# Optimization experiments

Measured on AMD Instinct MI355X. Metric: run time of the kernel, lower is better.

Reference implementation:

```python
import jax, jax.numpy as jnp
import numpy as np
from jax import lax

# Dims
HID = 2048          # hidden_size
DI = 4096           # d_inner = expand * hidden
NH = 64             # mamba heads
P = 64              # head dim
N = 128             # d_state
G = 1               # n_groups
K = 4               # conv kernel
IM = 8192           # MLP intermediate
BB, L = 2, 2048
EPS = 1e-5
CONV_DIM = DI + 2 * G * N            # 4352
D_IN_PROJ = 2 * DI + 2 * G * N + NH  # 8512


def rmsnorm(x, w, eps=EPS):
    v = jnp.mean(jnp.square(x), axis=-1, keepdims=True)
    return x * jax.lax.rsqrt(v + eps) * w


def setup_inputs() -> dict:
    key = jax.random.key(0)
    ks = jax.random.split(key, 16)
    s = 0.02
    return {
        "positions": jnp.broadcast_to(jnp.arange(L, dtype=jnp.int32), (BB, L)),
        "hidden_states": jax.random.normal(ks[0], (BB, L, HID), jnp.float32),
        "residual": jax.random.normal(ks[1], (BB, L, HID), jnp.float32),
        "in_proj_w": jax.random.normal(ks[2], (D_IN_PROJ, HID), jnp.float32) * s,
        "conv_w": jax.random.normal(ks[3], (CONV_DIM, K), jnp.float32) * 0.2,
        "conv_b": jax.random.normal(ks[4], (CONV_DIM,), jnp.float32) * 0.02,
        "A_log": jnp.log(jnp.arange(1, NH + 1, dtype=jnp.float32)),
        "D": jnp.ones((NH,), jnp.float32),
        "dt_bias": jax.random.uniform(ks[5], (NH,), jnp.float32, -4.0, -2.0),
        "mixer_norm_w": jnp.ones((DI,), jnp.float32),
        "out_proj_w": jax.random.normal(ks[6], (HID, DI), jnp.float32) * s,
        "input_ln_w": jnp.ones((HID,), jnp.float32),
        "pre_ff_ln_w": jnp.ones((HID,), jnp.float32),
        "gate_up_w": jax.random.normal(ks[7], (2 * IM, HID), jnp.float32) * s,
        "down_w": jax.random.normal(ks[8], (HID, IM), jnp.float32) * s,
    }


def reference(positions, hidden_states, residual, in_proj_w, conv_w, conv_b,
              A_log, D, dt_bias, mixer_norm_w, out_proj_w, input_ln_w,
              pre_ff_ln_w, gate_up_w, down_w):
    del positions  # not used by the mamba mixer math
    B_, Lq, _ = hidden_states.shape

    # --- input RMSNorm with fused residual add ---
    residual = hidden_states + residual
    hs = rmsnorm(residual, input_ln_w)

    # --- Mamba2 mixer ---
    proj = jnp.einsum('bld,ed->ble', hs, in_proj_w)   # [B,L,D_IN_PROJ]
    z = proj[..., :DI]
    xBC = proj[..., DI:DI + CONV_DIM]
    dt = proj[..., DI + CONV_DIM:]                    # [B,L,NH]

    # causal depthwise conv (kernel K) + SiLU
    xp = jnp.pad(xBC, ((0, 0), (K - 1, 0), (0, 0)))
    conv = conv_b
    for k in range(K):
        conv = conv + xp[:, k:k + Lq, :] * conv_w[:, k]
    xBC = jax.nn.silu(conv)

    x = xBC[..., :DI].reshape(B_, Lq, NH, P)
    Bm = xBC[..., DI:DI + G * N].reshape(B_, Lq, G, N)
    Cm = xBC[..., DI + G * N:].reshape(B_, Lq, G, N)
    rep = NH // G
    Bm = jnp.repeat(Bm, rep, axis=2)                  # [B,L,NH,N]
    Cm = jnp.repeat(Cm, rep, axis=2)

    dt = jax.nn.softplus(dt + dt_bias)                # [B,L,NH]
    A = -jnp.exp(A_log)                               # [NH]
    dA = jnp.exp(dt * A)                              # [B,L,NH]

    def step(h, inp):
        x_t, B_t, C_t, dA_t, dt_t = inp               # [B,NH,P],[B,NH,N],[B,NH,N],[B,NH],[B,NH]
        h = dA_t[..., None, None] * h + \
            (dt_t[..., None, None] * x_t[..., None]) * B_t[:, :, None, :]
        y = jnp.einsum('bhpn,bhn->bhp', h, C_t)
        return h, y

    xs = (x.transpose(1, 0, 2, 3), Bm.transpose(1, 0, 2, 3),
          Cm.transpose(1, 0, 2, 3), dA.transpose(1, 0, 2), dt.transpose(1, 0, 2))
    h0 = jnp.zeros((B_, NH, P, N), hidden_states.dtype)
    _, ys = lax.scan(step, h0, xs)                    # [L,B,NH,P]
    y = ys.transpose(1, 0, 2, 3) + D[None, None, :, None] * x
    y = y.reshape(B_, Lq, DI)

    # gated RMSNorm (Mixer2RMSNormGated, n_groups=1)
    y = y * jax.nn.silu(z)
    y = rmsnorm(y, mixer_norm_w)
    mamba_out = jnp.einsum('bld,hd->blh', y, out_proj_w)

    # --- pre-FF RMSNorm with fused residual add ---
    residual2 = mamba_out + residual
    hs2 = rmsnorm(residual2, pre_ff_ln_w)

    # --- gated MLP (SiluAndMul) ---
    gu = jnp.einsum('bld,ed->ble', hs2, gate_up_w)    # [B,L,2*IM]
    act = jax.nn.silu(gu[..., :IM]) * gu[..., IM:]
    out = jnp.einsum('bli,hi->blh', act, down_w)
    return out, residual2
```

## Files before the change

kernel.cpp:

```cpp
#include <hip/hip_runtime.h>

#define T_TOK 4096
#define HID   2048
#define DI    4096
#define NH    64
#define PDIM  64
#define NSTATE 128
#define IM    8192
#define LSEQ  2048
#define CONVD 4352
#define DPROJ 8512
#define DPADR 8704
#define QC    64
#define NCH   32

typedef __bf16 bf16x8 __attribute__((ext_vector_type(8)));
typedef float  f32x4  __attribute__((ext_vector_type(4)));

__device__ __forceinline__ unsigned short f2bf(float f) {
  unsigned u = __float_as_uint(f);
  u = (u + 0x7fffu + ((u >> 16) & 1u)) >> 16;
  return (unsigned short)u;
}
__device__ __forceinline__ float bf2f(unsigned short h) {
  return __uint_as_float(((unsigned)h) << 16);
}
__device__ __forceinline__ float siluf(float x) {
  return x / (1.f + __expf(-x));
}

#define GLL(gaddr, laddr) __builtin_amdgcn_global_load_lds( \
    (const __attribute__((address_space(1))) void*)(gaddr), \
    (__attribute__((address_space(3))) void*)(laddr), 16, 0, 0)

__global__ __launch_bounds__(256) void k_cvt(const float* __restrict__ src,
                                             unsigned short* __restrict__ dst, int n4) {
  int gid = blockIdx.x * 256 + threadIdx.x;
  if (gid >= n4) return;
  float4 v = *(const float4*)&src[(size_t)gid * 4];
  unsigned short* o = dst + (size_t)gid * 4;
  o[0] = f2bf(v.x); o[1] = f2bf(v.y); o[2] = f2bf(v.z); o[3] = f2bf(v.w);
}

__global__ __launch_bounds__(256) void k_cvt_inproj(const float* __restrict__ src,
                                                    unsigned short* __restrict__ dst) {
  int gid = blockIdx.x * 256 + threadIdx.x;
  size_t idx4 = (size_t)gid * 4;
  int r = (int)(idx4 >> 11);
  unsigned short* o = dst + idx4;
  if (r < DPROJ) {
    float4 v = *(const float4*)&src[(size_t)r * HID + (idx4 & 2047)];
    o[0] = f2bf(v.x); o[1] = f2bf(v.y); o[2] = f2bf(v.z); o[3] = f2bf(v.w);
  } else {
    o[0] = 0; o[1] = 0; o[2] = 0; o[3] = 0;
  }
}

__global__ __launch_bounds__(256) void k_cvt_gu(const float* __restrict__ src,
                                                unsigned short* __restrict__ dst) {
  int gid = blockIdx.x * 256 + threadIdx.x;
  size_t idx4 = (size_t)gid * 4;
  int r = (int)(idx4 >> 11), k = (int)(idx4 & 2047);
  int g = r >> 6, j = r & 63;
  int srcr = (j < 32) ? (g * 32 + j) : (IM + g * 32 + (j - 32));
  float4 v = *(const float4*)&src[(size_t)srcr * HID + k];
  unsigned short* o = dst + idx4;
  o[0] = f2bf(v.x); o[1] = f2bf(v.y); o[2] = f2bf(v.z); o[3] = f2bf(v.w);
}

template <int EPI, int BM>
__global__ __launch_bounds__(512, 2)
void gemm8(const unsigned short* __restrict__ A, const unsigned short* __restrict__ W,
           int K, int ntn, int ldo, void* __restrict__ outp,
           const float* __restrict__ resid) {
  (void)ntn;
  constexpr int MREP  = BM / 32;
  constexpr int ABYT  = BM * 128;
  constexpr int BUFB  = ABYT + 32768;
  constexpr int NTM   = 4096 / BM;
  __shared__ __align__(16) char smem[2 * BUFB];
  const int t = threadIdx.x;
  const int w = t >> 6, l = t & 63;
  const int lr = l & 15, hi = l >> 4;
  const int wr = w >> 2, wc = w & 3;

  const int q = (int)gridDim.x >> 3;
  const int bid = blockIdx.x;
  const int id2 = (bid & 7) * q + (bid >> 3);
  const int tn = id2 / NTM, tm = id2 % NTM;
  const int m0b = tm * BM, n0b = tn << 8;

  const int srow = t >> 3;
  const int scole = ((t & 7) << 3) ^ ((t & 32) ? 16 : 0) ^ ((t & 64) ? 32 : 0);
  const unsigned short* Ag = A + (size_t)(m0b + srow) * K + scole;
  const unsigned short* Wg = W + (size_t)(n0b + srow) * K + scole;
  const int ldsw = w * 1024;

  const int fa = ((lr & 4) ? 32 : 0) | ((lr & 8) ? 64 : 0);
  const int arow = (wr * (BM / 2) + lr) * 128 + hi * 16;
  const int brow = (wc * 64 + lr) * 128 + hi * 16;
  const int aoff0 = arow ^ fa, aoff1 = (arow + 64) ^ fa;
  const int boff0 = brow ^ fa, boff1 = (brow + 64) ^ fa;

#define ISSUE_A(jt, bb) do {                                                    \
    _Pragma("unroll")                                                           \
    for (int p_ = 0; p_ < BM / 64; ++p_)                                        \
      GLL(Ag + (size_t)(p_ * 64) * K + (size_t)(jt) * 64,                       \
          smem + (bb) * BUFB + p_ * 8192 + ldsw); } while (0)
#define ISSUE_B(jt, bb) do {                                                    \
    _Pragma("unroll")                                                           \
    for (int p_ = 0; p_ < 4; ++p_)                                              \
      GLL(Wg + (size_t)(p_ * 64) * K + (size_t)(jt) * 64,                       \
          smem + (bb) * BUFB + ABYT + p_ * 8192 + ldsw); } while (0)

#define RDF(off, base) (*(const bf16x8*)((base) + (off)))
#define MF(P, x, y, c0, c1, c2, c3) do {                                                     \
    __builtin_amdgcn_s_setprio(1);                                                           \
    acc[2*(P)  ][0] = __builtin_amdgcn_mfma_f32_16x16x32_bf16((x),(c0),acc[2*(P)  ][0],0,0,0);\
    acc[2*(P)+1][0] = __builtin_amdgcn_mfma_f32_16x16x32_bf16((y),(c0),acc[2*(P)+1][0],0,0,0);\
    acc[2*(P)  ][1] = __builtin_amdgcn_mfma_f32_16x16x32_bf16((x),(c1),acc[2*(P)  ][1],0,0,0);\
    acc[2*(P)+1][1] = __builtin_amdgcn_mfma_f32_16x16x32_bf16((y),(c1),acc[2*(P)+1][1],0,0,0);\
    acc[2*(P)  ][2] = __builtin_amdgcn_mfma_f32_16x16x32_bf16((x),(c2),acc[2*(P)  ][2],0,0,0);\
    acc[2*(P)+1][2] = __builtin_amdgcn_mfma_f32_16x16x32_bf16((y),(c2),acc[2*(P)+1][2],0,0,0);\
    acc[2*(P)  ][3] = __builtin_amdgcn_mfma_f32_16x16x32_bf16((x),(c3),acc[2*(P)  ][3],0,0,0);\
    acc[2*(P)+1][3] = __builtin_amdgcn_mfma_f32_16x16x32_bf16((y),(c3),acc[2*(P)+1][3],0,0,0);\
    __builtin_amdgcn_s_setprio(0); } while (0)

  f32x4 acc[MREP][4];
#pragma unroll
  for (int m = 0; m < MREP; m++)
#pragma unroll
    for (int n = 0; n < 4; n++) acc[m][n] = (f32x4){0.f, 0.f, 0.f, 0.f};

  const int nkt = K >> 6;
  ISSUE_A(0, 0); ISSUE_B(0, 0);

  for (int j = 0; j < nkt; ++j) {
    const int cur = j & 1;
    const char* Ab = smem + cur * BUFB;
    const char* Bb = Ab + ABYT;
    asm volatile("s_waitcnt vmcnt(0)" ::: "memory");
    __builtin_amdgcn_s_barrier();
    __builtin_amdgcn_sched_barrier(0);
    if (j + 1 < nkt) { ISSUE_A(j + 1, cur ^ 1); ISSUE_B(j + 1, cur ^ 1); }
    bf16x8 b0 = RDF(boff0, Bb), b1 = RDF(boff0 + 2048, Bb),
           b2 = RDF(boff0 + 4096, Bb), b3 = RDF(boff0 + 6144, Bb);
    bf16x8 af0 = RDF(aoff0, Ab), af1 = RDF(aoff0 + 2048, Ab);
    bf16x8 af2, af3, b4, b5, b6, b7;
    if constexpr (MREP == 8) {
      af2 = RDF(aoff0 + 4096, Ab); af3 = RDF(aoff0 + 6144, Ab);
      MF(0, af0, af1, b0, b1, b2, b3);
      af0 = RDF(aoff0 + 8192, Ab); af1 = RDF(aoff0 + 10240, Ab);
      MF(1, af2, af3, b0, b1, b2, b3);
      af2 = RDF(aoff0 + 12288, Ab); af3 = RDF(aoff0 + 14336, Ab);
      MF(2, af0, af1, b0, b1, b2, b3);
      b4 = RDF(boff1, Bb); b5 = RDF(boff1 + 2048, Bb);
      b6 = RDF(boff1 + 4096, Bb); b7 = RDF(boff1 + 6144, Bb);
      af0 = RDF(aoff1, Ab); af1 = RDF(aoff1 + 2048, Ab);
      MF(3, af2, af3, b0, b1, b2, b3);
      af2 = RDF(aoff1 + 4096, Ab); af3 = RDF(aoff1 + 6144, Ab);
      MF(0, af0, af1, b4, b5, b6, b7);
      af0 = RDF(aoff1 + 8192, Ab); af1 = RDF(aoff1 + 10240, Ab);
      MF(1, af2, af3, b4, b5, b6, b7);
      af2 = RDF(aoff1 + 12288, Ab); af3 = RDF(aoff1 + 14336, Ab);
      MF(2, af0, af1, b4, b5, b6, b7);
      MF(3, af2, af3, b4, b5, b6, b7);
    } else {
      af2 = RDF(aoff0 + 4096, Ab); af3 = RDF(aoff0 + 6144, Ab);
      MF(0, af0, af1, b0, b1, b2, b3);
      b4 = RDF(boff1, Bb); b5 = RDF(boff1 + 2048, Bb);
      b6 = RDF(boff1 + 4096, Bb); b7 = RDF(boff1 + 6144, Bb);
      af0 = RDF(aoff1, Ab); af1 = RDF(aoff1 + 2048, Ab);
      MF(1, af2, af3, b0, b1, b2, b3);
      af2 = RDF(aoff1 + 4096, Ab); af3 = RDF(aoff1 + 6144, Ab);
      MF(0, af0, af1, b4, b5, b6, b7);
      MF(1, af2, af3, b4, b5, b6, b7);
    }
  }

  if constexpr (EPI == 0) {
    unsigned short* op = (unsigned short*)outp;
#pragma unroll
    for (int m = 0; m < MREP; m++)
#pragma unroll
      for (int n = 0; n < 4; n++)
#pragma unroll
        for (int r = 0; r < 4; r++) {
          int row = m0b + wr * (BM / 2) + m * 16 + hi * 4 + r;
          int col = n0b + wc * 64 + n * 16 + lr;
          op[(size_t)row * ldo + col] = f2bf(acc[m][n][r]);
        }
  } else if constexpr (EPI == 2) {
    unsigned short* op = (unsigned short*)outp;
    const int gbase = (n0b + wc * 64) >> 1;
#pragma unroll
    for (int m = 0; m < MREP; m++)
#pragma unroll
      for (int n = 0; n < 2; n++)
#pragma unroll
        for (int r = 0; r < 4; r++) {
          int row = m0b + wr * (BM / 2) + m * 16 + hi * 4 + r;
          int col = gbase + n * 16 + lr;
          float g = acc[m][n][r], u = acc[m][n + 2][r];
          op[(size_t)row * ldo + col] = f2bf(siluf(g) * u);
        }
  } else {
    float* op = (float*)outp;
#pragma unroll
    for (int m = 0; m < MREP; m++)
#pragma unroll
      for (int n = 0; n < 4; n++)
#pragma unroll
        for (int r = 0; r < 4; r++) {
          int row = m0b + wr * (BM / 2) + m * 16 + hi * 4 + r;
          int col = n0b + wc * 64 + n * 16 + lr;
          float v = acc[m][n][r];
          if constexpr (EPI == 1) v += resid[(size_t)row * ldo + col];
          op[(size_t)row * ldo + col] = v;
        }
  }
#undef ISSUE_A
#undef ISSUE_B
#undef RDF
#undef MF
}

__device__ __forceinline__ float block_reduce_sum256(float v, float* sred) {
#pragma unroll
  for (int m = 32; m; m >>= 1) v += __shfl_xor(v, m);
  int t = threadIdx.x;
  if ((t & 63) == 0) sred[t >> 6] = v;
  __syncthreads();
  return sred[0] + sred[1] + sred[2] + sred[3];
}

__global__ __launch_bounds__(256)
void k_addnorm(const float* __restrict__ hin, const float* __restrict__ rin,
               const float* __restrict__ wln, float* __restrict__ rout,
               unsigned short* __restrict__ hbf) {
  __shared__ float sred[4];
  const int tok = blockIdx.x, t = threadIdx.x;
  const size_t base = (size_t)tok * HID + t * 8;
  float4 a0 = *(const float4*)&hin[base];
  float4 a1 = *(const float4*)&hin[base + 4];
  float4 b0 = *(const float4*)&rin[base];
  float4 b1 = *(const float4*)&rin[base + 4];
  float v[8] = {a0.x + b0.x, a0.y + b0.y, a0.z + b0.z, a0.w + b0.w,
                a1.x + b1.x, a1.y + b1.y, a1.z + b1.z, a1.w + b1.w};
  float ss = 0.f;
#pragma unroll
  for (int j = 0; j < 8; j++) ss += v[j] * v[j];
  float tot = block_reduce_sum256(ss, sred);
  float rms = rsqrtf(tot * (1.f / HID) + 1e-5f);
  *(float4*)&rout[base] = (float4){v[0], v[1], v[2], v[3]};
  *(float4*)&rout[base + 4] = (float4){v[4], v[5], v[6], v[7]};
  float4 w0 = *(const float4*)&wln[t * 8];
  float4 w1 = *(const float4*)&wln[t * 8 + 4];
  float wa[8] = {w0.x, w0.y, w0.z, w0.w, w1.x, w1.y, w1.z, w1.w};
  unsigned short o[8];
#pragma unroll
  for (int j = 0; j < 8; j++) o[j] = f2bf(v[j] * rms * wa[j]);
  *(ushort4*)&hbf[base] = *(ushort4*)&o[0];
  *(ushort4*)&hbf[base + 4] = *(ushort4*)&o[4];
}

__global__ __launch_bounds__(256)
void k_rmsnorm_bf(const float* __restrict__ src, const float* __restrict__ wln,
                  unsigned short* __restrict__ dst) {
  __shared__ float sred[4];
  const int tok = blockIdx.x, t = threadIdx.x;
  const size_t base = (size_t)tok * HID + t * 8;
  float4 a0 = *(const float4*)&src[base];
  float4 a1 = *(const float4*)&src[base + 4];
  float v[8] = {a0.x, a0.y, a0.z, a0.w, a1.x, a1.y, a1.z, a1.w};
  float ss = 0.f;
#pragma unroll
  for (int j = 0; j < 8; j++) ss += v[j] * v[j];
  float tot = block_reduce_sum256(ss, sred);
  float rms = rsqrtf(tot * (1.f / HID) + 1e-5f);
  float4 w0 = *(const float4*)&wln[t * 8];
  float4 w1 = *(const float4*)&wln[t * 8 + 4];
  float wa[8] = {w0.x, w0.y, w0.z, w0.w, w1.x, w1.y, w1.z, w1.w};
  unsigned short o[8];
#pragma unroll
  for (int j = 0; j < 8; j++) o[j] = f2bf(v[j] * rms * wa[j]);
  *(ushort4*)&dst[base] = *(ushort4*)&o[0];
  *(ushort4*)&dst[base + 4] = *(ushort4*)&o[4];
}

__global__ __launch_bounds__(256)
void k_gatenorm(const unsigned short* __restrict__ ybuf, const unsigned short* __restrict__ projbf,
                const float* __restrict__ wmix, unsigned short* __restrict__ ynorm) {
  __shared__ float sred[4];
  const int tok = blockIdx.x, t = threadIdx.x;
  const size_t yb = (size_t)tok * DI;
  const size_t pb = (size_t)tok * DPADR;
  float g[16];
  float ss = 0.f;
#pragma unroll
  for (int j = 0; j < 16; j++) {
    int idx = j * 256 + t;
    float yv = bf2f(ybuf[yb + idx]);
    float z = bf2f(projbf[pb + idx]);
    float gg = yv * siluf(z);
    g[j] = gg;
    ss += gg * gg;
  }
  float tot = block_reduce_sum256(ss, sred);
  float rms = rsqrtf(tot * (1.f / DI) + 1e-5f);
#pragma unroll
  for (int j = 0; j < 16; j++) {
    int idx = j * 256 + t;
    ynorm[yb + idx] = f2bf(g[j] * rms * wmix[idx]);
  }
}

__global__ __launch_bounds__(256)
void k_conv(const unsigned short* __restrict__ projbf, const float* __restrict__ cw,
            const float* __restrict__ cb, unsigned short* __restrict__ xbf,
            unsigned short* __restrict__ bcbf) {
  const int c = blockIdx.x * 256 + threadIdx.x;
  const int tk = blockIdx.y;
  const int lpos = tk & (LSEQ - 1);
  float4 wv = *(const float4*)&cw[c * 4];
  float wk[4] = {wv.x, wv.y, wv.z, wv.w};
  float acc = cb[c];
#pragma unroll
  for (int k = 0; k < 4; k++) {
    int lp = lpos - 3 + k;
    if (lp >= 0) acc += bf2f(projbf[(size_t)(tk - 3 + k) * DPADR + DI + c]) * wk[k];
  }
  unsigned short r = f2bf(siluf(acc));
  if (c < DI) xbf[(size_t)tk * DI + c] = r;
  else        bcbf[(size_t)tk * 256 + (c - DI)] = r;
}

__global__ __launch_bounds__(256)
void k_dt(const unsigned short* __restrict__ projbf, const float* __restrict__ dt_bias,
          float* __restrict__ dtg) {
  int gid = blockIdx.x * 256 + threadIdx.x;
  int tk = gid >> 6, hh = gid & 63;
  float x = bf2f(projbf[(size_t)tk * DPADR + (DI + CONVD) + hh]) + dt_bias[hh];
  float dt = (x > 20.f) ? x : log1pf(__expf(x));
  dtg[gid] = dt;
}

__global__ __launch_bounds__(256)
void k_ssd1(const unsigned short* __restrict__ xbf, const unsigned short* __restrict__ bcbf,
            const float* __restrict__ dtg, const float* __restrict__ A_log,
            const float* __restrict__ Dv, unsigned short* __restrict__ ybuf,
            unsigned short* __restrict__ Sc, float* __restrict__ dtsum) {
  __shared__ __align__(16) char smem[60928];
  unsigned short* sBs  = (unsigned short*)(smem);
  unsigned short* sCs  = (unsigned short*)(smem + 16384);
  unsigned short* sMs  = (unsigned short*)(smem + 16384);
  unsigned short* sBsT = (unsigned short*)(smem + 32768);
  unsigned short* sXsT = (unsigned short*)(smem + 51200);
  float* sdt = (float*)(smem + 60416);
  float* sdl = (float*)(smem + 60672);

  const int bi = blockIdx.x;
  const int ch = bi & 31, h = (bi >> 5) & 63, b = bi >> 11;
  const int bh = b * NH + h;
  const int tok0 = b * LSEQ + ch * QC;
  const int t = threadIdx.x;
  const int w = t >> 6, l = t & 63, lr = l & 15, hi = l >> 4;
  const float Ah = -__expf(A_log[h]);
  const float Dh = Dv[h];

  {
    const int srow = t >> 4, scol = (t & 15) * 8;
#pragma unroll
    for (int i = 0; i < 4; i++) {
      const unsigned short* gb = bcbf + (size_t)(tok0 + srow + 16 * i) * 256 + scol;
      GLL(gb, (char*)sBs + i * 4096 + w * 1024);
      GLL(gb + 128, (char*)sCs + i * 4096 + w * 1024);
    }
  }
  if (t < QC) sdt[t] = dtg[(size_t)(tok0 + t) * NH + h];
  __syncthreads();
  if (t < QC) sdl[t] = sdt[t];
  __syncthreads();
  for (int off = 1; off < QC; off <<= 1) {
    float v = 0.f;
    if (t < QC && t >= off) v = sdl[t - off];
    __syncthreads();
    if (t < QC) sdl[t] += v;
    __syncthreads();
  }

  {
    const int s = t >> 2;
    const float DlQ = sdl[QC - 1];
    const float csc = __expf(Ah * (DlQ - sdl[s])) * sdt[s];
    const int n0 = (t & 3) * 32;
#pragma unroll
    for (int j = 0; j < 32; j++) {
      float bv = bf2f(sBs[s * 128 + n0 + j]);
      sBsT[(n0 + j) * 72 + s] = f2bf(csc * bv);
    }
    const int p0 = (t & 3) * 16;
    const unsigned short* gx = xbf + (size_t)(tok0 + s) * DI + h * 64 + p0;
    union { uint4 v; unsigned short u[8]; } x0, x1;
    x0.v = *(const uint4*)gx;
    x1.v = *(const uint4*)(gx + 8);
#pragma unroll
    for (int j = 0; j < 8; j++) {
      sXsT[(p0 + j) * 72 + s] = x0.u[j];
      sXsT[(p0 + 8 + j) * 72 + s] = x1.u[j];
    }
  }
  __syncthreads();

  f32x4 accS[4];
#pragma unroll
  for (int jf = 0; jf < 4; jf++) accS[jf] = (f32x4){0.f, 0.f, 0.f, 0.f};
#pragma unroll
  for (int ks = 0; ks < 4; ks++) {
    bf16x8 a = *(const bf16x8*)&sBs[(w * 16 + lr) * 128 + ks * 32 + hi * 8];
#pragma unroll
    for (int jf = 0; jf < 4; jf++) {
      bf16x8 bb = *(const bf16x8*)&sCs[(jf * 16 + lr) * 128 + ks * 32 + hi * 8];
      accS[jf] = __builtin_amdgcn_mfma_f32_16x16x32_bf16(a, bb, accS[jf], 0, 0, 0);
    }
  }
  __syncthreads();

  {
    const int s0 = w * 16 + hi * 4;
#pragma unroll
    for (int jf = 0; jf < 4; jf++) {
      const int tt = jf * 16 + lr;
      const float dlt = sdl[tt];
      unsigned short mv[4];
#pragma unroll
      for (int r = 0; r < 4; r++) {
        const int ss = s0 + r;
        float val = 0.f;
        if (ss <= tt) val = accS[jf][r] * __expf(Ah * (dlt - sdl[ss])) * sdt[ss];
        mv[r] = f2bf(val);
      }
      *(ushort4*)&sMs[tt * 72 + s0] = *(ushort4*)mv;
    }
  }
  __syncthreads();

  {
    f32x4 accY[4];
#pragma unroll
    for (int jf = 0; jf < 4; jf++) accY[jf] = (f32x4){0.f, 0.f, 0.f, 0.f};
#pragma unroll
    for (int ks = 0; ks < 2; ks++) {
      bf16x8 a = *(const bf16x8*)&sMs[(w * 16 + lr) * 72 + ks * 32 + hi * 8];
#pragma unroll
      for (int jf = 0; jf < 4; jf++) {
        bf16x8 bb = *(const bf16x8*)&sXsT[(jf * 16 + lr) * 72 + ks * 32 + hi * 8];
        accY[jf] = __builtin_amdgcn_mfma_f32_16x16x32_bf16(a, bb, accY[jf], 0, 0, 0);
      }
    }
#pragma unroll
    for (int jf = 0; jf < 4; jf++)
#pragma unroll
      for (int r = 0; r < 4; r++) {
        const int tt = w * 16 + hi * 4 + r;
        const int pp = jf * 16 + lr;
        float xv = bf2f(sXsT[pp * 72 + tt]);
        ybuf[(size_t)(tok0 + tt) * DI + h * 64 + pp] = f2bf(accY[jf][r] + Dh * xv);
      }
  }

  {
    f32x4 accT[8];
#pragma unroll
    for (int jf = 0; jf < 8; jf++) accT[jf] = (f32x4){0.f, 0.f, 0.f, 0.f};
#pragma unroll
    for (int ks = 0; ks < 2; ks++) {
      bf16x8 a = *(const bf16x8*)&sXsT[(w * 16 + lr) * 72 + ks * 32 + hi * 8];
#pragma unroll
      for (int jf = 0; jf < 8; jf++) {
        bf16x8 bb = *(const bf16x8*)&sBsT[(jf * 16 + lr) * 72 + ks * 32 + hi * 8];
        accT[jf] = __builtin_amdgcn_mfma_f32_16x16x32_bf16(a, bb, accT[jf], 0, 0, 0);
      }
    }
    unsigned short* sc = Sc + ((size_t)bh * NCH + ch) * (PDIM * NSTATE);
#pragma unroll
    for (int jf = 0; jf < 8; jf++)
#pragma unroll
      for (int r = 0; r < 4; r++) {
        const int pp = w * 16 + hi * 4 + r;
        const int nn = jf * 16 + lr;
        sc[pp * NSTATE + nn] = f2bf(accT[jf][r]);
      }
  }
  if (t == 0) dtsum[bh * NCH + ch] = sdl[QC - 1];
}

__global__ __launch_bounds__(256)
void k_ssd2(const float* __restrict__ A_log, const float* __restrict__ dtsum,
            unsigned short* __restrict__ ScHt) {
  const int blk = blockIdx.x;
  const int bh = blk >> 3, pg = blk & 7;
  const int t = threadIdx.x;
  const int p = pg * 8 + (t >> 5), n0 = (t & 31) * 4;
  const int h = bh & 63;
  const float Ah = -__expf(A_log[h]);
  float H[4] = {0.f, 0.f, 0.f, 0.f};
  for (int c = 0; c < NCH; c++) {
    size_t base = (((size_t)bh * NCH + c) * PDIM + p) * NSTATE + n0;
    ushort4 sv = *(const ushort4*)&ScHt[base];
    float dec = __expf(Ah * dtsum[bh * NCH + c]);
    ushort4 hv;
    hv.x = f2bf(H[0]); hv.y = f2bf(H[1]); hv.z = f2bf(H[2]); hv.w = f2bf(H[3]);
    *(ushort4*)&ScHt[base] = hv;
    H[0] = dec * H[0] + bf2f(sv.x);
    H[1] = dec * H[1] + bf2f(sv.y);
    H[2] = dec * H[2] + bf2f(sv.z);
    H[3] = dec * H[3] + bf2f(sv.w);
  }
}

__global__ __launch_bounds__(256)
void k_ssd3(const unsigned short* __restrict__ bcbf, const unsigned short* __restrict__ Ht,
            const float* __restrict__ dtg, const float* __restrict__ A_log,
            unsigned short* __restrict__ ybuf) {
  __shared__ __align__(16) char smem[33280];
  unsigned short* sCs = (unsigned short*)(smem);
  unsigned short* sHt = (unsigned short*)(smem + 16384);
  float* sdt = (float*)(smem + 32768);
  float* sdl = (float*)(smem + 33024);

  const int bi = blockIdx.x;
  const int ch = bi & 31, h = (bi >> 5) & 63, b = bi >> 11;
  const int bh = b * NH + h;
  const int tok0 = b * LSEQ + ch * QC;
  const int t = threadIdx.x;
  const int w = t >> 6, l = t & 63, lr = l & 15, hi = l >> 4;
  const float Ah = -__expf(A_log[h]);

  {
    const int srow = t >> 4, scol = (t & 15) * 8;
    const unsigned short* gh = Ht + ((size_t)bh * NCH + ch) * (PDIM * NSTATE);
#pragma unroll
    for (int i = 0; i < 4; i++) {
      const unsigned short* gc = bcbf + (size_t)(tok0 + srow + 16 * i) * 256 + 128 + scol;
      GLL(gc, (char*)sCs + i * 4096 + w * 1024);
      GLL(gh + i * 2048 + t * 8, (char*)sHt + i * 4096 + w * 1024);
    }
  }
  if (t < QC) sdt[t] = dtg[(size_t)(tok0 + t) * NH + h];
  __syncthreads();
  if (t < QC) sdl[t] = sdt[t];
  __syncthreads();
  for (int off = 1; off < QC; off <<= 1) {
    float v = 0.f;
    if (t < QC && t >= off) v = sdl[t - off];
    __syncthreads();
    if (t < QC) sdl[t] += v;
    __syncthreads();
  }

  f32x4 acc[4];
#pragma unroll
  for (int jf = 0; jf < 4; jf++) acc[jf] = (f32x4){0.f, 0.f, 0.f, 0.f};
#pragma unroll
  for (int ks = 0; ks < 4; ks++) {
    bf16x8 a = *(const bf16x8*)&sCs[(w * 16 + lr) * 128 + ks * 32 + hi * 8];
#pragma unroll
    for (int jf = 0; jf < 4; jf++) {
      bf16x8 bb = *(const bf16x8*)&sHt[(jf * 16 + lr) * 128 + ks * 32 + hi * 8];
      acc[jf] = __builtin_amdgcn_mfma_f32_16x16x32_bf16(a, bb, acc[jf], 0, 0, 0);
    }
  }
#pragma unroll
  for (int jf = 0; jf < 4; jf++)
#pragma unroll
    for (int r = 0; r < 4; r++) {
      const int tt = w * 16 + hi * 4 + r;
      const int pp = jf * 16 + lr;
      const float dec = __expf(Ah * sdl[tt]);
      const size_t o = (size_t)(tok0 + tt) * DI + h * 64 + pp;
      ybuf[o] = f2bf(bf2f(ybuf[o]) + dec * acc[jf][r]);
    }
}

static const size_t OFF_WBF_IN  = 0;
static const size_t OFF_WBF_OUT = 35651584;
static const size_t OFF_WBF_GU  = 52428800;
static const size_t OFF_WBF_DN  = 119537664;
static const size_t OFF_RESID   = 153092096;
static const size_t OFF_HSBF    = 186646528;
static const size_t OFF_PROJ    = 203423744;
static const size_t OFF_XBF     = 274726912;
static const size_t OFF_BCBF    = 308281344;
static const size_t OFF_DTG     = 310378496;
static const size_t OFF_YBUF    = 311427072;
static const size_t OFF_SC      = 344981504;
static const size_t OFF_DTSUM   = 412090368;

extern "C" void kernel_launch(void* const* d_in, const int* in_sizes, int n_in,
                              void* d_out, int out_size, void* d_ws, size_t ws_size,
                              hipStream_t stream) {
  (void)in_sizes; (void)n_in; (void)out_size; (void)ws_size;
  const float* hidden   = (const float*)d_in[1];
  const float* resin    = (const float*)d_in[2];
  const float* w_inproj = (const float*)d_in[3];
  const float* conv_w   = (const float*)d_in[4];
  const float* conv_b   = (const float*)d_in[5];
  const float* A_log    = (const float*)d_in[6];
  const float* Dvec     = (const float*)d_in[7];
  const float* dt_bias  = (const float*)d_in[8];
  const float* w_mix    = (const float*)d_in[9];
  const float* w_outp   = (const float*)d_in[10];
  const float* w_ln1    = (const float*)d_in[11];
  const float* w_ln2    = (const float*)d_in[12];
  const float* w_gu     = (const float*)d_in[13];
  const float* w_dn     = (const float*)d_in[14];

  char* ws = (char*)d_ws;
  unsigned short* wbf_in  = (unsigned short*)(ws + OFF_WBF_IN);
  unsigned short* wbf_out = (unsigned short*)(ws + OFF_WBF_OUT);
  unsigned short* wbf_gu  = (unsigned short*)(ws + OFF_WBF_GU);
  unsigned short* wbf_dn  = (unsigned short*)(ws + OFF_WBF_DN);
  float*          residb  = (float*)(ws + OFF_RESID);
  unsigned short* hsbf    = (unsigned short*)(ws + OFF_HSBF);
  unsigned short* projbf  = (unsigned short*)(ws + OFF_PROJ);
  unsigned short* actbf   = (unsigned short*)(ws + OFF_PROJ);
  unsigned short* xbf     = (unsigned short*)(ws + OFF_XBF);
  unsigned short* ynormbf = (unsigned short*)(ws + OFF_XBF);
  unsigned short* bcbf    = (unsigned short*)(ws + OFF_BCBF);
  float*          dtgb    = (float*)(ws + OFF_DTG);
  unsigned short* ybuf    = (unsigned short*)(ws + OFF_YBUF);
  unsigned short* scht    = (unsigned short*)(ws + OFF_SC);
  float*          dtsumb  = (float*)(ws + OFF_DTSUM);

  float* out0 = (float*)d_out;
  float* res2 = out0 + (size_t)T_TOK * HID;

  k_cvt_inproj<<<17408, 256, 0, stream>>>(w_inproj, wbf_in);
  k_cvt<<<8192, 256, 0, stream>>>(w_outp, wbf_out, 2097152);
  k_cvt_gu<<<32768, 256, 0, stream>>>(w_gu, wbf_gu);
  k_cvt<<<16384, 256, 0, stream>>>(w_dn, wbf_dn, 4194304);

  k_addnorm<<<T_TOK, 256, 0, stream>>>(hidden, resin, w_ln1, residb, hsbf);
  gemm8<0, 256><<<34 * 16, 512, 0, stream>>>(hsbf, wbf_in, HID, 34, DPADR, projbf, nullptr);
  k_conv<<<dim3(17, T_TOK), 256, 0, stream>>>(projbf, conv_w, conv_b, xbf, bcbf);
  k_dt<<<T_TOK * NH / 256, 256, 0, stream>>>(projbf, dt_bias, dtgb);
  k_ssd1<<<4096, 256, 0, stream>>>(xbf, bcbf, dtgb, A_log, Dvec, ybuf, scht, dtsumb);
  k_ssd2<<<1024, 256, 0, stream>>>(A_log, dtsumb, scht);
  k_ssd3<<<4096, 256, 0, stream>>>(bcbf, scht, dtgb, A_log, ybuf);
  k_gatenorm<<<T_TOK, 256, 0, stream>>>(ybuf, projbf, w_mix, ynormbf);
  gemm8<1, 128><<<8 * 32, 512, 0, stream>>>(ynormbf, wbf_out, DI, 8, HID, res2, residb);
  k_rmsnorm_bf<<<T_TOK, 256, 0, stream>>>(res2, w_ln2, hsbf);
  gemm8<2, 256><<<64 * 16, 512, 0, stream>>>(hsbf, wbf_gu, HID, 64, IM, actbf, nullptr);
  gemm8<3, 128><<<8 * 32, 512, 0, stream>>>(actbf, wbf_dn, IM, 8, HID, out0, nullptr);
}
```

Before: 1.007 ms.

## Restructure GEMM main loop into barrier-separated phases with split global prefetch

The GEMM inner loop is rewritten into NQ phases per k-tile. In each phase the LDS fragment reads are issued first, then the next tile's global-to-LDS loads (A in the first phase, B in the second for the large tile), then a barrier and a block of MFMAs at raised priority, with the vmcnt wait deferred to the last phase. The aim is to keep waves in lockstep and spread memory issue across the compute so loads overlap with MFMA work better. In exchange it adds more barriers per k-tile and changes register pressure, since all eight B fragments are loaded up front.

Result: slower. 1.064 ms (+5.7%).

```diff
diff --git a/kernel.cpp b/kernel.cpp
--- a/kernel.cpp
+++ b/kernel.cpp
@@ -71,10 +71,10 @@
 template <int EPI, int BM>
 __global__ __launch_bounds__(512, 2)
 void gemm8(const unsigned short* __restrict__ A, const unsigned short* __restrict__ W,
-           int K, int ntn, int ldo, void* __restrict__ outp,
+           int K, int ldo, void* __restrict__ outp,
            const float* __restrict__ resid) {
-  (void)ntn;
   constexpr int MREP  = BM / 32;
+  constexpr int NQ    = MREP / 2;
   constexpr int ABYT  = BM * 128;
   constexpr int BUFB  = ABYT + 32768;
   constexpr int NTM   = 4096 / BM;
@@ -84,9 +84,9 @@
   const int lr = l & 15, hi = l >> 4;
   const int wr = w >> 2, wc = w & 3;
 
-  const int q = (int)gridDim.x >> 3;
+  const int q8 = (int)gridDim.x >> 3;
   const int bid = blockIdx.x;
-  const int id2 = (bid & 7) * q + (bid >> 3);
+  const int id2 = (bid & 7) * q8 + (bid >> 3);
   const int tn = id2 / NTM, tm = id2 % NTM;
   const int m0b = tm * BM, n0b = tn << 8;
 
@@ -114,17 +114,6 @@
           smem + (bb) * BUFB + ABYT + p_ * 8192 + ldsw); } while (0)
 
 #define RDF(off, base) (*(const bf16x8*)((base) + (off)))
-#define MF(P, x, y, c0, c1, c2, c3) do {                                                     \
-    __builtin_amdgcn_s_setprio(1);                                                           \
-    acc[2*(P)  ][0] = __builtin_amdgcn_mfma_f32_16x16x32_bf16((x),(c0),acc[2*(P)  ][0],0,0,0);\
-    acc[2*(P)+1][0] = __builtin_amdgcn_mfma_f32_16x16x32_bf16((y),(c0),acc[2*(P)+1][0],0,0,0);\
-    acc[2*(P)  ][1] = __builtin_amdgcn_mfma_f32_16x16x32_bf16((x),(c1),acc[2*(P)  ][1],0,0,0);\
-    acc[2*(P)+1][1] = __builtin_amdgcn_mfma_f32_16x16x32_bf16((y),(c1),acc[2*(P)+1][1],0,0,0);\
-    acc[2*(P)  ][2] = __builtin_amdgcn_mfma_f32_16x16x32_bf16((x),(c2),acc[2*(P)  ][2],0,0,0);\
-    acc[2*(P)+1][2] = __builtin_amdgcn_mfma_f32_16x16x32_bf16((y),(c2),acc[2*(P)+1][2],0,0,0);\
-    acc[2*(P)  ][3] = __builtin_amdgcn_mfma_f32_16x16x32_bf16((x),(c3),acc[2*(P)  ][3],0,0,0);\
-    acc[2*(P)+1][3] = __builtin_amdgcn_mfma_f32_16x16x32_bf16((y),(c3),acc[2*(P)+1][3],0,0,0);\
-    __builtin_amdgcn_s_setprio(0); } while (0)
 
   f32x4 acc[MREP][4];
 #pragma unroll
@@ -134,47 +123,51 @@
 
   const int nkt = K >> 6;
   ISSUE_A(0, 0); ISSUE_B(0, 0);
+  asm volatile("s_waitcnt vmcnt(0)" ::: "memory");
+  __builtin_amdgcn_s_barrier();
+  __builtin_amdgcn_sched_barrier(0);
 
   for (int j = 0; j < nkt; ++j) {
     const int cur = j & 1;
     const char* Ab = smem + cur * BUFB;
     const char* Bb = Ab + ABYT;
-    asm volatile("s_waitcnt vmcnt(0)" ::: "memory");
-    __builtin_amdgcn_s_barrier();
-    __builtin_amdgcn_sched_barrier(0);
-    if (j + 1 < nkt) { ISSUE_A(j + 1, cur ^ 1); ISSUE_B(j + 1, cur ^ 1); }
-    bf16x8 b0 = RDF(boff0, Bb), b1 = RDF(boff0 + 2048, Bb),
-           b2 = RDF(boff0 + 4096, Bb), b3 = RDF(boff0 + 6144, Bb);
-    bf16x8 af0 = RDF(aoff0, Ab), af1 = RDF(aoff0 + 2048, Ab);
-    bf16x8 af2, af3, b4, b5, b6, b7;
-    if constexpr (MREP == 8) {
-      af2 = RDF(aoff0 + 4096, Ab); af3 = RDF(aoff0 + 6144, Ab);
-      MF(0, af0, af1, b0, b1, b2, b3);
-      af0 = RDF(aoff0 + 8192, Ab); af1 = RDF(aoff0 + 10240, Ab);
-      MF(1, af2, af3, b0, b1, b2, b3);
-      af2 = RDF(aoff0 + 12288, Ab); af3 = RDF(aoff0 + 14336, Ab);
-      MF(2, af0, af1, b0, b1, b2, b3);
-      b4 = RDF(boff1, Bb); b5 = RDF(boff1 + 2048, Bb);
-      b6 = RDF(boff1 + 4096, Bb); b7 = RDF(boff1 + 6144, Bb);
-      af0 = RDF(aoff1, Ab); af1 = RDF(aoff1 + 2048, Ab);
-      MF(3, af2, af3, b0, b1, b2, b3);
-      af2 = RDF(aoff1 + 4096, Ab); af3 = RDF(aoff1 + 6144, Ab);
-      MF(0, af0, af1, b4, b5, b6, b7);
-      af0 = RDF(aoff1 + 8192, Ab); af1 = RDF(aoff1 + 10240, Ab);
-      MF(1, af2, af3, b4, b5, b6, b7);
-      af2 = RDF(aoff1 + 12288, Ab); af3 = RDF(aoff1 + 14336, Ab);
-      MF(2, af0, af1, b4, b5, b6, b7);
-      MF(3, af2, af3, b4, b5, b6, b7);
-    } else {
-      af2 = RDF(aoff0 + 4096, Ab); af3 = RDF(aoff0 + 6144, Ab);
-      MF(0, af0, af1, b0, b1, b2, b3);
-      b4 = RDF(boff1, Bb); b5 = RDF(boff1 + 2048, Bb);
-      b6 = RDF(boff1 + 4096, Bb); b7 = RDF(boff1 + 6144, Bb);
-      af0 = RDF(aoff1, Ab); af1 = RDF(aoff1 + 2048, Ab);
-      MF(1, af2, af3, b0, b1, b2, b3);
-      af2 = RDF(aoff1 + 4096, Ab); af3 = RDF(aoff1 + 6144, Ab);
-      MF(0, af0, af1, b4, b5, b6, b7);
-      MF(1, af2, af3, b4, b5, b6, b7);
+    bf16x8 bb[8];
+#pragma unroll
+    for (int q = 0; q < NQ; ++q) {
+      if (q == 0) {
+#pragma unroll
+        for (int n = 0; n < 4; n++) {
+          bb[n]     = RDF(boff0 + n * 2048, Bb);
+          bb[4 + n] = RDF(boff1 + n * 2048, Bb);
+        }
+      }
+      bf16x8 a0 = RDF(aoff0 + (2 * q) * 2048, Ab);
+      bf16x8 a1 = RDF(aoff0 + (2 * q + 1) * 2048, Ab);
+      bf16x8 a2 = RDF(aoff1 + (2 * q) * 2048, Ab);
+      bf16x8 a3 = RDF(aoff1 + (2 * q + 1) * 2048, Ab);
+      if (q == 0 && j + 1 < nkt) {
+        ISSUE_A(j + 1, cur ^ 1);
+        if (NQ == 2) ISSUE_B(j + 1, cur ^ 1);
+      }
+      if (q == 1 && NQ > 2 && j + 1 < nkt) ISSUE_B(j + 1, cur ^ 1);
+      __builtin_amdgcn_s_barrier();
+      __builtin_amdgcn_sched_barrier(0);
+      __builtin_amdgcn_s_setprio(1);
+#pragma unroll
+      for (int n = 0; n < 4; n++) {
+        acc[2 * q][n]     = __builtin_amdgcn_mfma_f32_16x16x32_bf16(a0, bb[n], acc[2 * q][n], 0, 0, 0);
+        acc[2 * q + 1][n] = __builtin_amdgcn_mfma_f32_16x16x32_bf16(a1, bb[n], acc[2 * q + 1][n], 0, 0, 0);
+      }
+#pragma unroll
+      for (int n = 0; n < 4; n++) {
+        acc[2 * q][n]     = __builtin_amdgcn_mfma_f32_16x16x32_bf16(a2, bb[4 + n], acc[2 * q][n], 0, 0, 0);
+        acc[2 * q + 1][n] = __builtin_amdgcn_mfma_f32_16x16x32_bf16(a3, bb[4 + n], acc[2 * q + 1][n], 0, 0, 0);
+      }
+      __builtin_amdgcn_s_setprio(0);
+      __builtin_amdgcn_sched_barrier(0);
+      if (q == NQ - 1) asm volatile("s_waitcnt vmcnt(0)" ::: "memory");
+      __builtin_amdgcn_s_barrier();
+      __builtin_amdgcn_sched_barrier(0);
     }
   }
 
@@ -222,7 +215,6 @@
 #undef ISSUE_A
 #undef ISSUE_B
 #undef RDF
-#undef MF
 }
 
 __device__ __forceinline__ float block_reduce_sum256(float v, float* sred) {
@@ -420,8 +412,8 @@
     bf16x8 a = *(const bf16x8*)&sBs[(w * 16 + lr) * 128 + ks * 32 + hi * 8];
 #pragma unroll
     for (int jf = 0; jf < 4; jf++) {
-      bf16x8 bb = *(const bf16x8*)&sCs[(jf * 16 + lr) * 128 + ks * 32 + hi * 8];
-      accS[jf] = __builtin_amdgcn_mfma_f32_16x16x32_bf16(a, bb, accS[jf], 0, 0, 0);
+      bf16x8 bbq = *(const bf16x8*)&sCs[(jf * 16 + lr) * 128 + ks * 32 + hi * 8];
+      accS[jf] = __builtin_amdgcn_mfma_f32_16x16x32_bf16(a, bbq, accS[jf], 0, 0, 0);
     }
   }
   __syncthreads();
@@ -454,8 +446,8 @@
       bf16x8 a = *(const bf16x8*)&sMs[(w * 16 + lr) * 72 + ks * 32 + hi * 8];
 #pragma unroll
       for (int jf = 0; jf < 4; jf++) {
-        bf16x8 bb = *(const bf16x8*)&sXsT[(jf * 16 + lr) * 72 + ks * 32 + hi * 8];
-        accY[jf] = __builtin_amdgcn_mfma_f32_16x16x32_bf16(a, bb, accY[jf], 0, 0, 0);
+        bf16x8 bbq = *(const bf16x8*)&sXsT[(jf * 16 + lr) * 72 + ks * 32 + hi * 8];
+        accY[jf] = __builtin_amdgcn_mfma_f32_16x16x32_bf16(a, bbq, accY[jf], 0, 0, 0);
       }
     }
 #pragma unroll
@@ -478,8 +470,8 @@
       bf16x8 a = *(const bf16x8*)&sXsT[(w * 16 + lr) * 72 + ks * 32 + hi * 8];
 #pragma unroll
       for (int jf = 0; jf < 8; jf++) {
-        bf16x8 bb = *(const bf16x8*)&sBsT[(jf * 16 + lr) * 72 + ks * 32 + hi * 8];
-        accT[jf] = __builtin_amdgcn_mfma_f32_16x16x32_bf16(a, bb, accT[jf], 0, 0, 0);
+        bf16x8 bbq = *(const bf16x8*)&sBsT[(jf * 16 + lr) * 72 + ks * 32 + hi * 8];
+        accT[jf] = __builtin_amdgcn_mfma_f32_16x16x32_bf16(a, bbq, accT[jf], 0, 0, 0);
       }
     }
     unsigned short* sc = Sc + ((size_t)bh * NCH + ch) * (PDIM * NSTATE);
@@ -567,8 +559,8 @@
     bf16x8 a = *(const bf16x8*)&sCs[(w * 16 + lr) * 128 + ks * 32 + hi * 8];
 #pragma unroll
     for (int jf = 0; jf < 4; jf++) {
-      bf16x8 bb = *(const bf16x8*)&sHt[(jf * 16 + lr) * 128 + ks * 32 + hi * 8];
-      acc[jf] = __builtin_amdgcn_mfma_f32_16x16x32_bf16(a, bb, acc[jf], 0, 0, 0);
+      bf16x8 bbq = *(const bf16x8*)&sHt[(jf * 16 + lr) * 128 + ks * 32 + hi * 8];
+      acc[jf] = __builtin_amdgcn_mfma_f32_16x16x32_bf16(a, bbq, acc[jf], 0, 0, 0);
     }
   }
 #pragma unroll
@@ -642,15 +634,15 @@
   k_cvt<<<16384, 256, 0, stream>>>(w_dn, wbf_dn, 4194304);
 
   k_addnorm<<<T_TOK, 256, 0, stream>>>(hidden, resin, w_ln1, residb, hsbf);
-  gemm8<0, 256><<<34 * 16, 512, 0, stream>>>(hsbf, wbf_in, HID, 34, DPADR, projbf, nullptr);
+  gemm8<0, 256><<<34 * 16, 512, 0, stream>>>(hsbf, wbf_in, HID, DPADR, projbf, nullptr);
   k_conv<<<dim3(17, T_TOK), 256, 0, stream>>>(projbf, conv_w, conv_b, xbf, bcbf);
   k_dt<<<T_TOK * NH / 256, 256, 0, stream>>>(projbf, dt_bias, dtgb);
   k_ssd1<<<4096, 256, 0, stream>>>(xbf, bcbf, dtgb, A_log, Dvec, ybuf, scht, dtsumb);
   k_ssd2<<<1024, 256, 0, stream>>>(A_log, dtsumb, scht);
   k_ssd3<<<4096, 256, 0, stream>>>(bcbf, scht, dtgb, A_log, ybuf);
   k_gatenorm<<<T_TOK, 256, 0, stream>>>(ybuf, projbf, w_mix, ynormbf);
-  gemm8<1, 128><<<8 * 32, 512, 0, stream>>>(ynormbf, wbf_out, DI, 8, HID, res2, residb);
+  gemm8<1, 128><<<8 * 32, 512, 0, stream>>>(ynormbf, wbf_out, DI, HID, res2, residb);
   k_rmsnorm_bf<<<T_TOK, 256, 0, stream>>>(res2, w_ln2, hsbf);
-  gemm8<2, 256><<<64 * 16, 512, 0, stream>>>(hsbf, wbf_gu, HID, 64, IM, actbf, nullptr);
-  gemm8<3, 128><<<8 * 32, 512, 0, stream>>>(actbf, wbf_dn, IM, 8, HID, out0, nullptr);
-}
+  gemm8<2, 256><<<64 * 16, 512, 0, stream>>>(hsbf, wbf_gu, HID, IM, actbf, nullptr);
+  gemm8<3, 128><<<8 * 32, 512, 0, stream>>>(actbf, wbf_dn, IM, HID, out0, nullptr);
+}
```
